# Kernel tuning notes

Measured on AMD Instinct MI355X. Metric: run time of the kernel, lower is better.

## Reference

```python
import jax, jax.numpy as jnp
import numpy as np

B, C, H, W = 8, 64, 64, 64
A = C // 8  # attention_dim = 8


def setup_inputs() -> dict:
    key = jax.random.key(0)
    ks = jax.random.split(key, 6)
    x = jax.random.normal(ks[0], (B, C, H, W), dtype=jnp.float32)
    # 1x1 conv weights as [out, in] matrices (kernel_size=1)
    Wq = jax.random.normal(ks[1], (A, C), dtype=jnp.float32) * 0.05
    bq = jnp.zeros((A,), dtype=jnp.float32)
    Wk = jax.random.normal(ks[2], (A, C), dtype=jnp.float32) * 0.05
    bk = jnp.zeros((A,), dtype=jnp.float32)
    Wv = jax.random.normal(ks[3], (C, C), dtype=jnp.float32) * 0.05
    bv = jnp.zeros((C,), dtype=jnp.float32)
    gamma = jnp.array(0.01, dtype=jnp.float32)  # nn.Parameter(ones(1)*0.01)
    ln_w = jnp.ones((C,), dtype=jnp.float32)
    ln_b = jnp.zeros((C,), dtype=jnp.float32)
    return {"x": x, "Wq": Wq, "bq": bq, "Wk": Wk, "bk": bk,
            "Wv": Wv, "bv": bv, "gamma": gamma, "ln_w": ln_w, "ln_b": ln_b}


def reference(x, Wq, bq, Wk, bk, Wv, bv, gamma, ln_w, ln_b):
    b, c, h, w = x.shape
    n = h * w
    xf = x.reshape(b, c, n)  # [B, C, N]
    # 1x1 convs == per-pixel channel GEMMs
    q = jnp.einsum('ac,bcn->ban', Wq, xf) + bq[None, :, None]  # [B, A, N]
    k = jnp.einsum('ac,bcn->ban', Wk, xf) + bk[None, :, None]  # [B, A, N]
    v = jnp.einsum('oc,bcn->bon', Wv, xf) + bv[None, :, None]  # [B, C, N]
    # energy[b,n,m] = <Q[:, n], K[:, m]>  (NO 1/sqrt(d) scaling, as in source)
    energy = jnp.einsum('ban,bam->bnm', q, k)  # [B, N, N]
    attention = jax.nn.softmax(energy, axis=-1)
    # bmm(V, attention^T): out[b,c,n] = sum_m attention[b,n,m] * V[b,c,m]
    attn_out = jnp.einsum('bnm,bcm->bcn', attention, v).reshape(b, c, h, w)
    feature_delta = gamma * attn_out
    pre_norm = feature_delta + x
    # LayerNorm over channel dim (channels-last in source)
    y = jnp.transpose(pre_norm, (0, 2, 3, 1))  # [B, H, W, C]
    mu = jnp.mean(y, axis=-1, keepdims=True)
    var = jnp.var(y, axis=-1, keepdims=True)
    yn = (y - mu) * jax.lax.rsqrt(var + 1e-5) * ln_w + ln_b
    out = jnp.transpose(yn, (0, 3, 1, 2))  # [B, C, H, W]
    return (out, attention, feature_delta, attn_out)
```

## Files before the change

kernel.cpp:

```cpp
#include <hip/hip_runtime.h>

#define NPIX 4096
#define CCH  64

typedef __attribute__((ext_vector_type(8))) short bf16x8;
typedef __attribute__((ext_vector_type(4))) float f32x4;

static __device__ __forceinline__ unsigned short f2bf(float f) {
    union { float f; unsigned u; } v; v.f = f;
    return (unsigned short)((v.u + 0x7FFFu + ((v.u >> 16) & 1u)) >> 16);
}
static __device__ __forceinline__ float bf2f_lo(unsigned u) {
    union { unsigned u; float f; } v; v.u = u << 16; return v.f;
}
static __device__ __forceinline__ float bf2f_hi(unsigned u) {
    union { unsigned u; float f; } v; v.u = u & 0xFFFF0000u; return v.f;
}


__global__ __launch_bounds__(256) void qkv_kernel(
    const float* __restrict__ x,
    const float* __restrict__ Wq, const float* __restrict__ bq,
    const float* __restrict__ Wk, const float* __restrict__ bk,
    const float* __restrict__ Wv, const float* __restrict__ bv,
    unsigned short* __restrict__ ws)
{
    __shared__ float xs[64][64];
    const int t  = threadIdx.x;
    const int b  = blockIdx.x >> 6;
    const int n0 = (blockIdx.x & 63) << 6;
    const float* xb = x + ((size_t)b * CCH) * NPIX;

    #pragma unroll
    for (int ii = 0; ii < 16; ++ii) {
        int idx = t + (ii << 8);
        int c = idx >> 6, nl = idx & 63;
        xs[c][nl] = xb[(size_t)c * NPIX + n0 + nl];
    }
    __syncthreads();

    const int nl = t & 63;
    const int og = t >> 6;
    unsigned short* qf = ws;
    unsigned short* kf = ws + 262144;
    unsigned short* vf = ws + 524288;
    const int n = n0 + nl;

    for (int oo = 0; oo < 20; ++oo) {
        const int o = og * 20 + oo;
        const float* Wrow;
        float bias;
        if (o < 8)       { Wrow = Wq + o * CCH;        bias = bq[o]; }
        else if (o < 16) { Wrow = Wk + (o - 8) * CCH;  bias = bk[o - 8]; }
        else             { Wrow = Wv + (o - 16) * CCH; bias = bv[o - 16]; }
        float acc = bias;
        #pragma unroll
        for (int c = 0; c < CCH; ++c) acc += Wrow[c] * xs[c][nl];
        if (o < 8)       qf[((size_t)b * NPIX + n) * 8 + o] = f2bf(acc);
        else if (o < 16) kf[((size_t)b * NPIX + n) * 8 + (o - 8)] = f2bf(acc);
        else {
            const int c  = o - 16;
            const int kc = n >> 5, r5 = n & 31;
            const int lane = ((r5 >> 3) << 4) | (c & 15);
            const size_t idx = ((((size_t)b * 128 + kc) * 4 + (c >> 4)) * 64 + lane) * 8 + (r5 & 7);
            vf[idx] = f2bf(acc);
        }
    }
}

__global__ __launch_bounds__(256) void attn_kernel(
    const float* __restrict__ x, const unsigned short* __restrict__ ws,
    const float* __restrict__ gamma_p,
    const float* __restrict__ ln_w, const float* __restrict__ ln_b,
    float* __restrict__ out, float* __restrict__ attn,
    float* __restrict__ fd_out, float* __restrict__ ao_out)
{
    __shared__ __align__(16) char psb0[16384];
    __shared__ __align__(16) char psb1[16384];
    __shared__ float rinv[32];

    const int bid = blockIdx.x;
    const int wg  = ((bid & 7) << 7) | (bid >> 3);
    const int b   = wg >> 7;
    const int n0  = (wg & 127) << 5;

    const unsigned short* qf = ws;
    const unsigned short* kf = ws + 262144;
    const unsigned short* vf = ws + 524288;

    const int t   = threadIdx.x;
    const int l   = t & 63;
    const int w   = t >> 6;
    const int g   = l >> 4;
    const int c16 = l & 15;

    const unsigned short* qfb = qf + ((size_t)b * NPIX + n0) * 8;
    const unsigned short* kfb = kf + (size_t)b * NPIX * 8;
    const unsigned short* vwave = vf + (size_t)b * 128 * 2048 + w * 512;

    const f32x4 zf = {0.f, 0.f, 0.f, 0.f};

    bf16x8 QB0 = {}, QB1 = {};
    if (l < 16) {
        QB0 = *(const bf16x8*)(qfb + l * 8);
        QB1 = *(const bf16x8*)(qfb + (16 + l) * 8);
    }

    float s0 = 0.f, s1 = 0.f;
    #pragma unroll 4
    for (int mt = 0; mt < 64; ++mt) {
        const int mbase = (w << 10) + (mt << 4);
        bf16x8 Kf = {};
        if (l < 16) Kf = *(const bf16x8*)(kfb + (size_t)(mbase + l) * 8);
        f32x4 e0 = __builtin_amdgcn_mfma_f32_16x16x32_bf16(Kf, QB0, zf, 0, 0, 0);
        f32x4 e1 = __builtin_amdgcn_mfma_f32_16x16x32_bf16(Kf, QB1, zf, 0, 0, 0);
        #pragma unroll
        for (int r = 0; r < 4; ++r) {
            s0 += __expf(e0[r]);
            s1 += __expf(e1[r]);
        }
    }
    s0 += __shfl_xor(s0, 16); s0 += __shfl_xor(s0, 32);
    s1 += __shfl_xor(s1, 16); s1 += __shfl_xor(s1, 32);
    {
        float* sred = (float*)psb0;
        if (l < 16) {
            sred[w * 32 + l]      = s0;
            sred[w * 32 + 16 + l] = s1;
        }
        __syncthreads();
        if (t < 32) {
            const float s = sred[t] + sred[32 + t] + sred[64 + t] + sred[96 + t];
            rinv[t] = 1.f / s;
        }
        __syncthreads();
    }
    const float ri0 = rinv[c16], ri1 = rinv[16 + c16];

    const int swx = (c16 & 7) << 4;
    const int wjg = (w << 7) + (g << 3);
    const int srow = (w << 3) + (l >> 3);
    const int ssw  = (srow & 7) << 4;
    const int srm  = (l & 7) << 3;
    float* attn_base = attn + ((size_t)b * NPIX + n0) * NPIX;
    float* arow = attn_base + (size_t)srow * NPIX + ((l & 7) << 2);

    f32x4 acc0 = zf, acc1 = zf;

#define PHASE_A(MC, BUF) do {                                                     \
    _Pragma("unroll")                                                             \
    for (int j = 0; j < 4; ++j) {                                                 \
        const int mg = ((MC) << 8) + (w << 6) + (j << 4);                         \
        bf16x8 Kf = {};                                                           \
        if (l < 16) Kf = *(const bf16x8*)(kfb + (size_t)(mg + l) * 8);            \
        f32x4 e0 = __builtin_amdgcn_mfma_f32_16x16x32_bf16(Kf, QB0, zf, 0, 0, 0); \
        f32x4 e1 = __builtin_amdgcn_mfma_f32_16x16x32_bf16(Kf, QB1, zf, 0, 0, 0); \
        uint2 pk0, pk1;                                                           \
        pk0.x = (unsigned)f2bf(__expf(e0[0]) * ri0) | ((unsigned)f2bf(__expf(e0[1]) * ri0) << 16); \
        pk0.y = (unsigned)f2bf(__expf(e0[2]) * ri0) | ((unsigned)f2bf(__expf(e0[3]) * ri0) << 16); \
        pk1.x = (unsigned)f2bf(__expf(e1[0]) * ri1) | ((unsigned)f2bf(__expf(e1[1]) * ri1) << 16); \
        pk1.y = (unsigned)f2bf(__expf(e1[2]) * ri1) | ((unsigned)f2bf(__expf(e1[3]) * ri1) << 16); \
        const int wo = (wjg + (j << 5)) ^ swx;                                    \
        *(uint2*)((BUF) + c16 * 512 + wo)        = pk0;                           \
        *(uint2*)((BUF) + (16 + c16) * 512 + wo) = pk1;                           \
    }                                                                             \
} while (0)

#define PHASE_B(MC, BUF) do {                                                     \
    const unsigned short* vbase = vwave + ((size_t)(MC) << 14);                   \
    __builtin_amdgcn_s_setprio(1);                                                \
    _Pragma("unroll")                                                             \
    for (int kc8 = 0; kc8 < 8; ++kc8) {                                           \
        const int aoff = ((kc8 << 6) | (g << 4)) ^ swx;                           \
        const bf16x8 Bf = *(const bf16x8*)(vbase + (size_t)kc8 * 2048 + l * 8);   \
        const bf16x8 A0 = *(const bf16x8*)((BUF) + c16 * 512 + aoff);             \
        const bf16x8 A1 = *(const bf16x8*)((BUF) + c16 * 512 + 8192 + aoff);      \
        acc0 = __builtin_amdgcn_mfma_f32_16x16x32_bf16(A0, Bf, acc0, 0, 0, 0);    \
        acc1 = __builtin_amdgcn_mfma_f32_16x16x32_bf16(A1, Bf, acc1, 0, 0, 0);    \
    }                                                                             \
    __builtin_amdgcn_s_setprio(0);                                                \
} while (0)

#define PHASE_S(MC, BUF) do {                                                     \
    _Pragma("unroll")                                                             \
    for (int i = 0; i < 8; ++i) {                                                 \
        const int ro = (srm + (i << 6)) ^ ssw;                                    \
        const uint2 rv = *(const uint2*)((BUF) + srow * 512 + ro);                \
        f32x4 fv;                                                                 \
        fv[0] = bf2f_lo(rv.x); fv[1] = bf2f_hi(rv.x);                             \
        fv[2] = bf2f_lo(rv.y); fv[3] = bf2f_hi(rv.y);                             \
        __builtin_nontemporal_store(fv, (f32x4*)(arow + ((MC) << 8) + (i << 5))); \
    }                                                                             \
} while (0)

    PHASE_A(0, psb0);
    __syncthreads();
    #pragma unroll 2
    for (int mc = 0; mc < 16; ++mc) {
        char* cur = (mc & 1) ? psb1 : psb0;
        char* nxt = (mc & 1) ? psb0 : psb1;
        if (mc < 15) PHASE_A(mc + 1, nxt);
        PHASE_B(mc, cur);
        PHASE_S(mc, cur);
        __syncthreads();
    }

    float* O_lds = (float*)psb0;
    float* muv   = (float*)(psb0 + 8448);
    float* rsg   = (float*)(psb0 + 8576);
    {
        const int ch = (w << 4) + c16;
        const int r0 = g << 2;
        #pragma unroll
        for (int r = 0; r < 4; ++r) {
            O_lds[ch * 33 + r0 + r]      = acc0[r];
            O_lds[ch * 33 + 16 + r0 + r] = acc1[r];
        }
    }
    __syncthreads();

    const float gma = gamma_p[0];
    const float* xb = x + (size_t)b * CCH * NPIX + n0;
    {
        const int r = t >> 3, l8 = t & 7;
        float sum = 0.f, sum2 = 0.f;
        #pragma unroll
        for (int cc = 0; cc < 8; ++cc) {
            const int c = l8 + (cc << 3);
            const float pre = xb[(size_t)c * NPIX + r] + gma * O_lds[c * 33 + r];
            sum += pre; sum2 += pre * pre;
        }
        #pragma unroll
        for (int off = 1; off < 8; off <<= 1) {
            sum  += __shfl_xor(sum, off);
            sum2 += __shfl_xor(sum2, off);
        }
        if (l8 == 0) {
            const float m_ = sum * (1.f / 64.f);
            const float v_ = sum2 * (1.f / 64.f) - m_ * m_;
            muv[r] = m_;
            rsg[r] = rsqrtf(v_ + 1e-5f);
        }
    }
    __syncthreads();

    #pragma unroll
    for (int ii = 0; ii < 8; ++ii) {
        const int idx = t + (ii << 8);
        const int c = idx >> 5, nl = idx & 31;
        const float o   = O_lds[c * 33 + nl];
        const float fdv = gma * o;
        const float pre = xb[(size_t)c * NPIX + nl] + fdv;
        const float y   = (pre - muv[nl]) * rsg[nl] * ln_w[c] + ln_b[c];
        const size_t off = (size_t)b * CCH * NPIX + (size_t)c * NPIX + n0 + nl;
        ao_out[off] = o;
        fd_out[off] = fdv;
        out[off]    = y;
    }
}

extern "C" void kernel_launch(void* const* d_in, const int* in_sizes, int n_in,
                              void* d_out, int out_size, void* d_ws, size_t ws_size,
                              hipStream_t stream) {
    const float* x     = (const float*)d_in[0];
    const float* Wq    = (const float*)d_in[1];
    const float* bq    = (const float*)d_in[2];
    const float* Wk    = (const float*)d_in[3];
    const float* bk    = (const float*)d_in[4];
    const float* Wv    = (const float*)d_in[5];
    const float* bv    = (const float*)d_in[6];
    const float* gamma = (const float*)d_in[7];
    const float* lnw   = (const float*)d_in[8];
    const float* lnb   = (const float*)d_in[9];

    float* out  = (float*)d_out;
    float* attn = out + 2097152;
    float* fd   = out + 136314880;
    float* ao   = out + 138412032;
    unsigned short* ws = (unsigned short*)d_ws;

    qkv_kernel<<<512, 256, 0, stream>>>(x, Wq, bq, Wk, bk, Wv, bv, ws);
    attn_kernel<<<1024, 256, 0, stream>>>(x, ws, gamma, lnw, lnb, out, attn, fd, ao);
}
```

Measured before the change: 171.0 us.

## Halve query rows per attention block to double grid size; cache x column in registers

The attention kernel now handles 16 query rows per block instead of 32, launching 2048 blocks with half the LDS footprint. The softmax, P·V, attention-store and LayerNorm epilogue indexing are all rewritten for the smaller tile. The aim is more blocks and waves in flight to keep the memory-bound attention-matrix stores saturated. The cost is that K and V fragments are re-read twice as often and each block issues fewer MFMAs per K load. Separately, the QKV kernel loads its x column into registers once instead of reading LDS in every output loop.

```diff
diff --git a/kernel.cpp b/kernel.cpp
--- a/kernel.cpp
+++ b/kernel.cpp
@@ -46,6 +46,10 @@
     unsigned short* vf = ws + 524288;
     const int n = n0 + nl;
 
+    float xr[64];
+    #pragma unroll
+    for (int c = 0; c < 64; ++c) xr[c] = xs[c][nl];
+
     for (int oo = 0; oo < 20; ++oo) {
         const int o = og * 20 + oo;
         const float* Wrow;
@@ -55,7 +59,7 @@
         else             { Wrow = Wv + (o - 16) * CCH; bias = bv[o - 16]; }
         float acc = bias;
         #pragma unroll
-        for (int c = 0; c < CCH; ++c) acc += Wrow[c] * xs[c][nl];
+        for (int c = 0; c < CCH; ++c) acc += Wrow[c] * xr[c];
         if (o < 8)       qf[((size_t)b * NPIX + n) * 8 + o] = f2bf(acc);
         else if (o < 16) kf[((size_t)b * NPIX + n) * 8 + (o - 8)] = f2bf(acc);
         else {
@@ -75,14 +79,14 @@
     float* __restrict__ out, float* __restrict__ attn,
     float* __restrict__ fd_out, float* __restrict__ ao_out)
 {
-    __shared__ __align__(16) char psb0[16384];
-    __shared__ __align__(16) char psb1[16384];
-    __shared__ float rinv[32];
+    __shared__ __align__(16) char psb0[8192];
+    __shared__ __align__(16) char psb1[8192];
+    __shared__ float rinv[16];
 
     const int bid = blockIdx.x;
-    const int wg  = ((bid & 7) << 7) | (bid >> 3);
-    const int b   = wg >> 7;
-    const int n0  = (wg & 127) << 5;
+    const int wg  = ((bid & 7) << 8) | (bid >> 3);
+    const int b   = wg >> 8;
+    const int n0  = (wg & 255) << 4;
 
     const unsigned short* qf = ws;
     const unsigned short* kf = ws + 262144;
@@ -100,52 +104,35 @@
 
     const f32x4 zf = {0.f, 0.f, 0.f, 0.f};
 
-    bf16x8 QB0 = {}, QB1 = {};
-    if (l < 16) {
-        QB0 = *(const bf16x8*)(qfb + l * 8);
-        QB1 = *(const bf16x8*)(qfb + (16 + l) * 8);
-    }
-
-    float s0 = 0.f, s1 = 0.f;
+    bf16x8 QB0 = {};
+    if (l < 16) QB0 = *(const bf16x8*)(qfb + l * 8);
+
+    float s0 = 0.f;
     #pragma unroll 4
     for (int mt = 0; mt < 64; ++mt) {
         const int mbase = (w << 10) + (mt << 4);
         bf16x8 Kf = {};
         if (l < 16) Kf = *(const bf16x8*)(kfb + (size_t)(mbase + l) * 8);
         f32x4 e0 = __builtin_amdgcn_mfma_f32_16x16x32_bf16(Kf, QB0, zf, 0, 0, 0);
-        f32x4 e1 = __builtin_amdgcn_mfma_f32_16x16x32_bf16(Kf, QB1, zf, 0, 0, 0);
-        #pragma unroll
-        for (int r = 0; r < 4; ++r) {
-            s0 += __expf(e0[r]);
-            s1 += __expf(e1[r]);
-        }
+        #pragma unroll
+        for (int r = 0; r < 4; ++r) s0 += __expf(e0[r]);
     }
     s0 += __shfl_xor(s0, 16); s0 += __shfl_xor(s0, 32);
-    s1 += __shfl_xor(s1, 16); s1 += __shfl_xor(s1, 32);
     {
         float* sred = (float*)psb0;
-        if (l < 16) {
-            sred[w * 32 + l]      = s0;
-            sred[w * 32 + 16 + l] = s1;
-        }
+        if (l < 16) sred[(w << 4) + l] = s0;
         __syncthreads();
-        if (t < 32) {
-            const float s = sred[t] + sred[32 + t] + sred[64 + t] + sred[96 + t];
-            rinv[t] = 1.f / s;
-        }
+        if (t < 16) rinv[t] = 1.f / (sred[t] + sred[16 + t] + sred[32 + t] + sred[48 + t]);
         __syncthreads();
     }
-    const float ri0 = rinv[c16], ri1 = rinv[16 + c16];
-
-    const int swx = (c16 & 7) << 4;
-    const int wjg = (w << 7) + (g << 3);
-    const int srow = (w << 3) + (l >> 3);
+    const float ri0 = rinv[c16];
+
+    const int swx  = (c16 & 7) << 4;
+    const int srow = t >> 4;
     const int ssw  = (srow & 7) << 4;
-    const int srm  = (l & 7) << 3;
-    float* attn_base = attn + ((size_t)b * NPIX + n0) * NPIX;
-    float* arow = attn_base + (size_t)srow * NPIX + ((l & 7) << 2);
-
-    f32x4 acc0 = zf, acc1 = zf;
+    float* arow = attn + ((size_t)b * NPIX + n0 + srow) * NPIX + ((t & 15) << 2);
+
+    f32x4 acc0 = zf;
 
 #define PHASE_A(MC, BUF) do {                                                     \
     _Pragma("unroll")                                                             \
@@ -154,15 +141,11 @@
         bf16x8 Kf = {};                                                           \
         if (l < 16) Kf = *(const bf16x8*)(kfb + (size_t)(mg + l) * 8);            \
         f32x4 e0 = __builtin_amdgcn_mfma_f32_16x16x32_bf16(Kf, QB0, zf, 0, 0, 0); \
-        f32x4 e1 = __builtin_amdgcn_mfma_f32_16x16x32_bf16(Kf, QB1, zf, 0, 0, 0); \
-        uint2 pk0, pk1;                                                           \
+        uint2 pk0;                                                                \
         pk0.x = (unsigned)f2bf(__expf(e0[0]) * ri0) | ((unsigned)f2bf(__expf(e0[1]) * ri0) << 16); \
         pk0.y = (unsigned)f2bf(__expf(e0[2]) * ri0) | ((unsigned)f2bf(__expf(e0[3]) * ri0) << 16); \
-        pk1.x = (unsigned)f2bf(__expf(e1[0]) * ri1) | ((unsigned)f2bf(__expf(e1[1]) * ri1) << 16); \
-        pk1.y = (unsigned)f2bf(__expf(e1[2]) * ri1) | ((unsigned)f2bf(__expf(e1[3]) * ri1) << 16); \
-        const int wo = (wjg + (j << 5)) ^ swx;                                    \
-        *(uint2*)((BUF) + c16 * 512 + wo)        = pk0;                           \
-        *(uint2*)((BUF) + (16 + c16) * 512 + wo) = pk1;                           \
+        const int wo = ((w << 7) + (j << 5) + (g << 3)) ^ swx;                    \
+        *(uint2*)((BUF) + c16 * 512 + wo) = pk0;                                  \
     }                                                                             \
 } while (0)
 
@@ -174,22 +157,20 @@
         const int aoff = ((kc8 << 6) | (g << 4)) ^ swx;                           \
         const bf16x8 Bf = *(const bf16x8*)(vbase + (size_t)kc8 * 2048 + l * 8);   \
         const bf16x8 A0 = *(const bf16x8*)((BUF) + c16 * 512 + aoff);             \
-        const bf16x8 A1 = *(const bf16x8*)((BUF) + c16 * 512 + 8192 + aoff);      \
         acc0 = __builtin_amdgcn_mfma_f32_16x16x32_bf16(A0, Bf, acc0, 0, 0, 0);    \
-        acc1 = __builtin_amdgcn_mfma_f32_16x16x32_bf16(A1, Bf, acc1, 0, 0, 0);    \
     }                                                                             \
     __builtin_amdgcn_s_setprio(0);                                                \
 } while (0)
 
 #define PHASE_S(MC, BUF) do {                                                     \
     _Pragma("unroll")                                                             \
-    for (int i = 0; i < 8; ++i) {                                                 \
-        const int ro = (srm + (i << 6)) ^ ssw;                                    \
+    for (int i = 0; i < 4; ++i) {                                                 \
+        const int ro = (((t & 15) << 3) + (i << 7)) ^ ssw;                        \
         const uint2 rv = *(const uint2*)((BUF) + srow * 512 + ro);                \
         f32x4 fv;                                                                 \
         fv[0] = bf2f_lo(rv.x); fv[1] = bf2f_hi(rv.x);                             \
         fv[2] = bf2f_lo(rv.y); fv[3] = bf2f_hi(rv.y);                             \
-        __builtin_nontemporal_store(fv, (f32x4*)(arow + ((MC) << 8) + (i << 5))); \
+        __builtin_nontemporal_store(fv, (f32x4*)(arow + ((MC) << 8) + (i << 6))); \
     }                                                                             \
 } while (0)
 
@@ -206,52 +187,49 @@
     }
 
     float* O_lds = (float*)psb0;
-    float* muv   = (float*)(psb0 + 8448);
-    float* rsg   = (float*)(psb0 + 8576);
+    float* muq   = (float*)psb1;
+    float* rsq   = (float*)(psb1 + 64);
     {
         const int ch = (w << 4) + c16;
         const int r0 = g << 2;
         #pragma unroll
-        for (int r = 0; r < 4; ++r) {
-            O_lds[ch * 33 + r0 + r]      = acc0[r];
-            O_lds[ch * 33 + 16 + r0 + r] = acc1[r];
-        }
+        for (int r = 0; r < 4; ++r) O_lds[ch * 17 + r0 + r] = acc0[r];
     }
     __syncthreads();
 
     const float gma = gamma_p[0];
     const float* xb = x + (size_t)b * CCH * NPIX + n0;
     {
-        const int r = t >> 3, l8 = t & 7;
+        const int r = t >> 4, l16 = t & 15;
         float sum = 0.f, sum2 = 0.f;
         #pragma unroll
-        for (int cc = 0; cc < 8; ++cc) {
-            const int c = l8 + (cc << 3);
-            const float pre = xb[(size_t)c * NPIX + r] + gma * O_lds[c * 33 + r];
+        for (int cc = 0; cc < 4; ++cc) {
+            const int c = l16 + (cc << 4);
+            const float pre = xb[(size_t)c * NPIX + r] + gma * O_lds[c * 17 + r];
             sum += pre; sum2 += pre * pre;
         }
         #pragma unroll
-        for (int off = 1; off < 8; off <<= 1) {
+        for (int off = 1; off < 16; off <<= 1) {
             sum  += __shfl_xor(sum, off);
             sum2 += __shfl_xor(sum2, off);
         }
-        if (l8 == 0) {
+        if (l16 == 0) {
             const float m_ = sum * (1.f / 64.f);
             const float v_ = sum2 * (1.f / 64.f) - m_ * m_;
-            muv[r] = m_;
-            rsg[r] = rsqrtf(v_ + 1e-5f);
+            muq[r] = m_;
+            rsq[r] = rsqrtf(v_ + 1e-5f);
         }
     }
     __syncthreads();
 
     #pragma unroll
-    for (int ii = 0; ii < 8; ++ii) {
+    for (int ii = 0; ii < 4; ++ii) {
         const int idx = t + (ii << 8);
-        const int c = idx >> 5, nl = idx & 31;
-        const float o   = O_lds[c * 33 + nl];
+        const int c = idx >> 4, nl = idx & 15;
+        const float o   = O_lds[c * 17 + nl];
         const float fdv = gma * o;
         const float pre = xb[(size_t)c * NPIX + nl] + fdv;
-        const float y   = (pre - muv[nl]) * rsg[nl] * ln_w[c] + ln_b[c];
+        const float y   = (pre - muq[nl]) * rsq[nl] * ln_w[c] + ln_b[c];
         const size_t off = (size_t)b * CCH * NPIX + (size_t)c * NPIX + n0 + nl;
         ao_out[off] = o;
         fd_out[off] = fdv;
@@ -280,5 +258,5 @@
     unsigned short* ws = (unsigned short*)d_ws;
 
     qkv_kernel<<<512, 256, 0, stream>>>(x, Wq, bq, Wk, bk, Wv, bv, ws);
-    attn_kernel<<<1024, 256, 0, stream>>>(x, ws, gamma, lnw, lnb, out, attn, fd, ao);
-}
+    attn_kernel<<<2048, 256, 0, stream>>>(x, ws, gamma, lnw, lnb, out, attn, fd, ao);
+}
```

Result: slower. 182.8 us (+6.9%).

## Store fp32 attention directly from MFMA results instead of via LDS roundtrip

Applied to the files above, without the earlier changes.

The attention matrix is now written to global memory straight from the exp results in phase A, with the full fp32 values, instead of being read back from the bf16 LDS tile in a separate store phase. This removes the LDS reread and bf16-to-fp32 conversion. It also makes the stored attention exact fp32 rather than bf16-rounded. In exchange, each lane writes 16-byte chunks scattered across 32 rows, so the global writes coalesce less well than the old row-contiguous stores. The change also caches x in registers in the QKV kernel, computes the softmax reciprocals per lane without an extra LDS array, and sets a minimum-blocks-per-CU hint on the attention kernel.

```diff
diff --git a/kernel.cpp b/kernel.cpp
--- a/kernel.cpp
+++ b/kernel.cpp
@@ -9,12 +9,6 @@
 static __device__ __forceinline__ unsigned short f2bf(float f) {
     union { float f; unsigned u; } v; v.f = f;
     return (unsigned short)((v.u + 0x7FFFu + ((v.u >> 16) & 1u)) >> 16);
-}
-static __device__ __forceinline__ float bf2f_lo(unsigned u) {
-    union { unsigned u; float f; } v; v.u = u << 16; return v.f;
-}
-static __device__ __forceinline__ float bf2f_hi(unsigned u) {
-    union { unsigned u; float f; } v; v.u = u & 0xFFFF0000u; return v.f;
 }
 
 
@@ -46,6 +40,10 @@
     unsigned short* vf = ws + 524288;
     const int n = n0 + nl;
 
+    float xr[64];
+    #pragma unroll
+    for (int c = 0; c < 64; ++c) xr[c] = xs[c][nl];
+
     for (int oo = 0; oo < 20; ++oo) {
         const int o = og * 20 + oo;
         const float* Wrow;
@@ -55,7 +53,7 @@
         else             { Wrow = Wv + (o - 16) * CCH; bias = bv[o - 16]; }
         float acc = bias;
         #pragma unroll
-        for (int c = 0; c < CCH; ++c) acc += Wrow[c] * xs[c][nl];
+        for (int c = 0; c < CCH; ++c) acc += Wrow[c] * xr[c];
         if (o < 8)       qf[((size_t)b * NPIX + n) * 8 + o] = f2bf(acc);
         else if (o < 16) kf[((size_t)b * NPIX + n) * 8 + (o - 8)] = f2bf(acc);
         else {
@@ -68,7 +66,7 @@
     }
 }
 
-__global__ __launch_bounds__(256) void attn_kernel(
+__global__ __launch_bounds__(256, 5) void attn_kernel(
     const float* __restrict__ x, const unsigned short* __restrict__ ws,
     const float* __restrict__ gamma_p,
     const float* __restrict__ ln_w, const float* __restrict__ ln_b,
@@ -77,7 +75,6 @@
 {
     __shared__ __align__(16) char psb0[16384];
     __shared__ __align__(16) char psb1[16384];
-    __shared__ float rinv[32];
 
     const int bid = blockIdx.x;
     const int wg  = ((bid & 7) << 7) | (bid >> 3);
@@ -122,28 +119,21 @@
     }
     s0 += __shfl_xor(s0, 16); s0 += __shfl_xor(s0, 32);
     s1 += __shfl_xor(s1, 16); s1 += __shfl_xor(s1, 32);
+    float ri0, ri1;
     {
         float* sred = (float*)psb0;
         if (l < 16) {
-            sred[w * 32 + l]      = s0;
-            sred[w * 32 + 16 + l] = s1;
+            sred[(w << 5) + l]      = s0;
+            sred[(w << 5) + 16 + l] = s1;
         }
         __syncthreads();
-        if (t < 32) {
-            const float s = sred[t] + sred[32 + t] + sred[64 + t] + sred[96 + t];
-            rinv[t] = 1.f / s;
-        }
+        ri0 = 1.f / (sred[c16]      + sred[32 + c16]      + sred[64 + c16]      + sred[96 + c16]);
+        ri1 = 1.f / (sred[16 + c16] + sred[48 + c16]      + sred[80 + c16]      + sred[112 + c16]);
         __syncthreads();
     }
-    const float ri0 = rinv[c16], ri1 = rinv[16 + c16];
 
     const int swx = (c16 & 7) << 4;
-    const int wjg = (w << 7) + (g << 3);
-    const int srow = (w << 3) + (l >> 3);
-    const int ssw  = (srow & 7) << 4;
-    const int srm  = (l & 7) << 3;
     float* attn_base = attn + ((size_t)b * NPIX + n0) * NPIX;
-    float* arow = attn_base + (size_t)srow * NPIX + ((l & 7) << 2);
 
     f32x4 acc0 = zf, acc1 = zf;
 
@@ -155,12 +145,22 @@
         if (l < 16) Kf = *(const bf16x8*)(kfb + (size_t)(mg + l) * 8);            \
         f32x4 e0 = __builtin_amdgcn_mfma_f32_16x16x32_bf16(Kf, QB0, zf, 0, 0, 0); \
         f32x4 e1 = __builtin_amdgcn_mfma_f32_16x16x32_bf16(Kf, QB1, zf, 0, 0, 0); \
+        f32x4 p0, p1;                                                             \
+        _Pragma("unroll")                                                         \
+        for (int r = 0; r < 4; ++r) {                                             \
+            p0[r] = __expf(e0[r]) * ri0;                                          \
+            p1[r] = __expf(e1[r]) * ri1;                                          \
+        }                                                                         \
+        __builtin_nontemporal_store(p0,                                           \
+            (f32x4*)(attn_base + (size_t)c16 * NPIX + mg + (g << 2)));            \
+        __builtin_nontemporal_store(p1,                                           \
+            (f32x4*)(attn_base + (size_t)(16 + c16) * NPIX + mg + (g << 2)));     \
         uint2 pk0, pk1;                                                           \
-        pk0.x = (unsigned)f2bf(__expf(e0[0]) * ri0) | ((unsigned)f2bf(__expf(e0[1]) * ri0) << 16); \
-        pk0.y = (unsigned)f2bf(__expf(e0[2]) * ri0) | ((unsigned)f2bf(__expf(e0[3]) * ri0) << 16); \
-        pk1.x = (unsigned)f2bf(__expf(e1[0]) * ri1) | ((unsigned)f2bf(__expf(e1[1]) * ri1) << 16); \
-        pk1.y = (unsigned)f2bf(__expf(e1[2]) * ri1) | ((unsigned)f2bf(__expf(e1[3]) * ri1) << 16); \
-        const int wo = (wjg + (j << 5)) ^ swx;                                    \
+        pk0.x = (unsigned)f2bf(p0[0]) | ((unsigned)f2bf(p0[1]) << 16);            \
+        pk0.y = (unsigned)f2bf(p0[2]) | ((unsigned)f2bf(p0[3]) << 16);            \
+        pk1.x = (unsigned)f2bf(p1[0]) | ((unsigned)f2bf(p1[1]) << 16);            \
+        pk1.y = (unsigned)f2bf(p1[2]) | ((unsigned)f2bf(p1[3]) << 16);            \
+        const int wo = ((w << 7) + (j << 5) + (g << 3)) ^ swx;                    \
         *(uint2*)((BUF) + c16 * 512 + wo)        = pk0;                           \
         *(uint2*)((BUF) + (16 + c16) * 512 + wo) = pk1;                           \
     }                                                                             \
@@ -181,18 +181,6 @@
     __builtin_amdgcn_s_setprio(0);                                                \
 } while (0)
 
-#define PHASE_S(MC, BUF) do {                                                     \
-    _Pragma("unroll")                                                             \
-    for (int i = 0; i < 8; ++i) {                                                 \
-        const int ro = (srm + (i << 6)) ^ ssw;                                    \
-        const uint2 rv = *(const uint2*)((BUF) + srow * 512 + ro);                \
-        f32x4 fv;                                                                 \
-        fv[0] = bf2f_lo(rv.x); fv[1] = bf2f_hi(rv.x);                             \
-        fv[2] = bf2f_lo(rv.y); fv[3] = bf2f_hi(rv.y);                             \
-        __builtin_nontemporal_store(fv, (f32x4*)(arow + ((MC) << 8) + (i << 5))); \
-    }                                                                             \
-} while (0)
-
     PHASE_A(0, psb0);
     __syncthreads();
     #pragma unroll 2
@@ -201,9 +189,10 @@
         char* nxt = (mc & 1) ? psb0 : psb1;
         if (mc < 15) PHASE_A(mc + 1, nxt);
         PHASE_B(mc, cur);
-        PHASE_S(mc, cur);
         __syncthreads();
     }
+#undef PHASE_A
+#undef PHASE_B
 
     float* O_lds = (float*)psb0;
     float* muv   = (float*)(psb0 + 8448);
```

Result: slower. 219.1 us (+28.1%).

## Use exp2 with log-sum offset, prefetch K fragments, cache x in registers

Applied to the files above, without the earlier changes.

Pre-scales Q by log2(e) so softmax exponentials use the native exp2 instruction, and turns normalisation into an additive -log2(sum) inside the exponent instead of a multiply by a reciprocal. K fragments for score chunks are prefetched into registers two chunks ahead through a ping-pong register buffer, taking global loads off the dependent path. The QKV projection caches each pixel's 64-channel column in registers rather than rereading LDS for every output. The attention kernel gets a minimum-occupancy launch bound, which may constrain register allocation.

```diff
diff --git a/kernel.cpp b/kernel.cpp
--- a/kernel.cpp
+++ b/kernel.cpp
@@ -2,6 +2,7 @@
 
 #define NPIX 4096
 #define CCH  64
+#define LOG2E 1.44269504088896f
 
 typedef __attribute__((ext_vector_type(8))) short bf16x8;
 typedef __attribute__((ext_vector_type(4))) float f32x4;
@@ -46,6 +47,10 @@
     unsigned short* vf = ws + 524288;
     const int n = n0 + nl;
 
+    float xr[64];
+    #pragma unroll
+    for (int c = 0; c < 64; ++c) xr[c] = xs[c][nl];
+
     for (int oo = 0; oo < 20; ++oo) {
         const int o = og * 20 + oo;
         const float* Wrow;
@@ -55,8 +60,8 @@
         else             { Wrow = Wv + (o - 16) * CCH; bias = bv[o - 16]; }
         float acc = bias;
         #pragma unroll
-        for (int c = 0; c < CCH; ++c) acc += Wrow[c] * xs[c][nl];
-        if (o < 8)       qf[((size_t)b * NPIX + n) * 8 + o] = f2bf(acc);
+        for (int c = 0; c < CCH; ++c) acc += Wrow[c] * xr[c];
+        if (o < 8)       qf[((size_t)b * NPIX + n) * 8 + o] = f2bf(acc * LOG2E);
         else if (o < 16) kf[((size_t)b * NPIX + n) * 8 + (o - 8)] = f2bf(acc);
         else {
             const int c  = o - 16;
@@ -68,7 +73,7 @@
     }
 }
 
-__global__ __launch_bounds__(256) void attn_kernel(
+__global__ __launch_bounds__(256, 5) void attn_kernel(
     const float* __restrict__ x, const unsigned short* __restrict__ ws,
     const float* __restrict__ gamma_p,
     const float* __restrict__ ln_w, const float* __restrict__ ln_b,
@@ -77,7 +82,6 @@
 {
     __shared__ __align__(16) char psb0[16384];
     __shared__ __align__(16) char psb1[16384];
-    __shared__ float rinv[32];
 
     const int bid = blockIdx.x;
     const int wg  = ((bid & 7) << 7) | (bid >> 3);
@@ -105,6 +109,20 @@
         QB0 = *(const bf16x8*)(qfb + l * 8);
         QB1 = *(const bf16x8*)(qfb + (16 + l) * 8);
     }
+
+    bf16x8 KrA[4] = {}, KrB[4] = {};
+
+#define KLOAD(MC, KR) do {                                                        \
+    if (l < 16) {                                                                 \
+        _Pragma("unroll")                                                         \
+        for (int j = 0; j < 4; ++j) {                                             \
+            const int mg = ((MC) << 8) + (w << 6) + (j << 4);                     \
+            KR[j] = *(const bf16x8*)(kfb + (size_t)(mg + l) * 8);                 \
+        }                                                                         \
+    }                                                                             \
+} while (0)
+
+    KLOAD(0, KrA);
 
     float s0 = 0.f, s1 = 0.f;
     #pragma unroll 4
@@ -116,51 +134,50 @@
         f32x4 e1 = __builtin_amdgcn_mfma_f32_16x16x32_bf16(Kf, QB1, zf, 0, 0, 0);
         #pragma unroll
         for (int r = 0; r < 4; ++r) {
-            s0 += __expf(e0[r]);
-            s1 += __expf(e1[r]);
+            s0 += __builtin_amdgcn_exp2f(e0[r]);
+            s1 += __builtin_amdgcn_exp2f(e1[r]);
         }
     }
     s0 += __shfl_xor(s0, 16); s0 += __shfl_xor(s0, 32);
     s1 += __shfl_xor(s1, 16); s1 += __shfl_xor(s1, 32);
+    float lr0, lr1;
     {
         float* sred = (float*)psb0;
         if (l < 16) {
-            sred[w * 32 + l]      = s0;
-            sred[w * 32 + 16 + l] = s1;
+            sred[(w << 5) + l]      = s0;
+            sred[(w << 5) + 16 + l] = s1;
         }
         __syncthreads();
-        if (t < 32) {
-            const float s = sred[t] + sred[32 + t] + sred[64 + t] + sred[96 + t];
-            rinv[t] = 1.f / s;
-        }
+        const float st0 = sred[c16]      + sred[32 + c16] + sred[64 + c16] + sred[96 + c16];
+        const float st1 = sred[16 + c16] + sred[48 + c16] + sred[80 + c16] + sred[112 + c16];
+        lr0 = -__builtin_amdgcn_logf(st0);
+        lr1 = -__builtin_amdgcn_logf(st1);
         __syncthreads();
     }
-    const float ri0 = rinv[c16], ri1 = rinv[16 + c16];
-
-    const int swx = (c16 & 7) << 4;
-    const int wjg = (w << 7) + (g << 3);
+
+    const int swx  = (c16 & 7) << 4;
     const int srow = (w << 3) + (l >> 3);
     const int ssw  = (srow & 7) << 4;
     const int srm  = (l & 7) << 3;
-    float* attn_base = attn + ((size_t)b * NPIX + n0) * NPIX;
-    float* arow = attn_base + (size_t)srow * NPIX + ((l & 7) << 2);
+    float* arow = attn + ((size_t)b * NPIX + n0 + srow) * NPIX + ((l & 7) << 2);
 
     f32x4 acc0 = zf, acc1 = zf;
 
-#define PHASE_A(MC, BUF) do {                                                     \
+#define PHASE_A(BUF, KR) do {                                                     \
     _Pragma("unroll")                                                             \
     for (int j = 0; j < 4; ++j) {                                                 \
-        const int mg = ((MC) << 8) + (w << 6) + (j << 4);                         \
-        bf16x8 Kf = {};                                                           \
-        if (l < 16) Kf = *(const bf16x8*)(kfb + (size_t)(mg + l) * 8);            \
-        f32x4 e0 = __builtin_amdgcn_mfma_f32_16x16x32_bf16(Kf, QB0, zf, 0, 0, 0); \
-        f32x4 e1 = __builtin_amdgcn_mfma_f32_16x16x32_bf16(Kf, QB1, zf, 0, 0, 0); \
+        f32x4 e0 = __builtin_amdgcn_mfma_f32_16x16x32_bf16(KR[j], QB0, zf, 0, 0, 0); \
+        f32x4 e1 = __builtin_amdgcn_mfma_f32_16x16x32_bf16(KR[j], QB1, zf, 0, 0, 0); \
         uint2 pk0, pk1;                                                           \
-        pk0.x = (unsigned)f2bf(__expf(e0[0]) * ri0) | ((unsigned)f2bf(__expf(e0[1]) * ri0) << 16); \
-        pk0.y = (unsigned)f2bf(__expf(e0[2]) * ri0) | ((unsigned)f2bf(__expf(e0[3]) * ri0) << 16); \
-        pk1.x = (unsigned)f2bf(__expf(e1[0]) * ri1) | ((unsigned)f2bf(__expf(e1[1]) * ri1) << 16); \
-        pk1.y = (unsigned)f2bf(__expf(e1[2]) * ri1) | ((unsigned)f2bf(__expf(e1[3]) * ri1) << 16); \
-        const int wo = (wjg + (j << 5)) ^ swx;                                    \
+        pk0.x = (unsigned)f2bf(__builtin_amdgcn_exp2f(e0[0] + lr0))               \
+              | ((unsigned)f2bf(__builtin_amdgcn_exp2f(e0[1] + lr0)) << 16);      \
+        pk0.y = (unsigned)f2bf(__builtin_amdgcn_exp2f(e0[2] + lr0))               \
+              | ((unsigned)f2bf(__builtin_amdgcn_exp2f(e0[3] + lr0)) << 16);      \
+        pk1.x = (unsigned)f2bf(__builtin_amdgcn_exp2f(e1[0] + lr1))               \
+              | ((unsigned)f2bf(__builtin_amdgcn_exp2f(e1[1] + lr1)) << 16);      \
+        pk1.y = (unsigned)f2bf(__builtin_amdgcn_exp2f(e1[2] + lr1))               \
+              | ((unsigned)f2bf(__builtin_amdgcn_exp2f(e1[3] + lr1)) << 16);      \
+        const int wo = ((w << 7) + (j << 5) + (g << 3)) ^ swx;                    \
         *(uint2*)((BUF) + c16 * 512 + wo)        = pk0;                           \
         *(uint2*)((BUF) + (16 + c16) * 512 + wo) = pk1;                           \
     }                                                                             \
@@ -193,17 +210,26 @@
     }                                                                             \
 } while (0)
 
-    PHASE_A(0, psb0);
+#define ITER(MC, CUR, NXT, KC, KN) do {                                           \
+    if ((MC) < 14) KLOAD((MC) + 2, KC);                                           \
+    if ((MC) < 15) PHASE_A(NXT, KN);                                              \
+    PHASE_B(MC, CUR);                                                             \
+    PHASE_S(MC, CUR);                                                             \
+    __syncthreads();                                                              \
+} while (0)
+
+    KLOAD(1, KrB);
+    PHASE_A(psb0, KrA);
     __syncthreads();
-    #pragma unroll 2
-    for (int mc = 0; mc < 16; ++mc) {
-        char* cur = (mc & 1) ? psb1 : psb0;
-        char* nxt = (mc & 1) ? psb0 : psb1;
-        if (mc < 15) PHASE_A(mc + 1, nxt);
-        PHASE_B(mc, cur);
-        PHASE_S(mc, cur);
-        __syncthreads();
-    }
+    for (int mc2 = 0; mc2 < 16; mc2 += 2) {
+        ITER(mc2,     psb0, psb1, KrA, KrB);
+        ITER(mc2 + 1, psb1, psb0, KrB, KrA);
+    }
+#undef KLOAD
+#undef PHASE_A
+#undef PHASE_B
+#undef PHASE_S
+#undef ITER
 
     float* O_lds = (float*)psb0;
     float* muv   = (float*)(psb0 + 8448);
```

Result: slower. 260.8 us (+52.5%).
